# Optimization experiments

Measured on AMD Instinct MI355X. Metric: run time of the kernel, lower is better.

The kernel has to match this reference:

```python
import jax, jax.numpy as jnp
import numpy as np

EPS = 1e-5
NUM_HEADS = 4
TEMP = 0.1


def setup_inputs() -> dict:
    key = jax.random.key(0)
    ks = jax.random.split(key, 12)
    n, c, s, p, k = 64, 256, 64, 16, 4
    sc = 1.0 / np.sqrt(c)
    return {
        "x": jax.random.normal(ks[0], (n, c, s, p), dtype=jnp.float32),
        "prototypes": jax.random.normal(ks[1], (p, k, c), dtype=jnp.float32),
        "Wq": jax.random.normal(ks[2], (c, c), dtype=jnp.float32) * sc,
        "bq": jnp.zeros((c,), dtype=jnp.float32),
        "Wk": jax.random.normal(ks[3], (c, c), dtype=jnp.float32) * sc,
        "bk": jnp.zeros((c,), dtype=jnp.float32),
        "Wv": jax.random.normal(ks[4], (c, c), dtype=jnp.float32) * sc,
        "bv": jnp.zeros((c,), dtype=jnp.float32),
        "Wo": jax.random.normal(ks[5], (c, c), dtype=jnp.float32) * sc,
        "bo": jnp.zeros((c,), dtype=jnp.float32),
        "fc_bin": jax.random.normal(ks[6], (p, k * c, c), dtype=jnp.float32) * (1.0 / np.sqrt(k * c)),
    }


def _causal_attention(x, Wq, bq, Wk, bk, Wv, bv, Wo, bo):
    # x: (B, S, C) -> multi-head causal self-attention
    B, S, C = x.shape
    H = NUM_HEADS
    D = C // H
    q = (x @ Wq + bq).reshape(B, S, H, D).transpose(0, 2, 1, 3)
    k = (x @ Wk + bk).reshape(B, S, H, D).transpose(0, 2, 1, 3)
    v = (x @ Wv + bv).reshape(B, S, H, D).transpose(0, 2, 1, 3)
    scores = jnp.einsum('bhqd,bhkd->bhqk', q, k) / jnp.sqrt(jnp.float32(D))
    causal = jnp.tril(jnp.ones((S, S), dtype=bool))
    scores = jnp.where(causal, scores, jnp.finfo(scores.dtype).min)
    attn = jax.nn.softmax(scores, axis=-1)
    out = jnp.einsum('bhqk,bhkd->bhqd', attn, v)
    out = out.transpose(0, 2, 1, 3).reshape(B, S, C)
    return out @ Wo + bo


def reference(x, prototypes, Wq, bq, Wk, bk, Wv, bv, Wo, bo, fc_bin):
    n, c, s, p = x.shape
    kclusters = prototypes.shape[1]
    # n c s p -> p n s c
    x_part = x.transpose(3, 0, 2, 1)
    # InstanceNorm1d over the temporal (s) axis per (p, n, c)
    mu = x_part.mean(axis=2, keepdims=True)
    var = x_part.var(axis=2, keepdims=True)
    x_normed = (x_part - mu) / jnp.sqrt(var + EPS)
    # cosine similarity with prototypes
    xn = x_normed / jnp.linalg.norm(x_normed, axis=-1, keepdims=True)
    pn = prototypes / jnp.linalg.norm(prototypes, axis=-1, keepdims=True)
    sim = jnp.einsum('pnsc,pkc->pnsk', xn, pn)
    # straight-through hard/soft assignment (training=True path)
    soft = jax.nn.softmax(sim / TEMP, axis=-1)
    hard_idx = jnp.argmax(soft, axis=-1)                      # (p, n, s)
    hard = jax.nn.one_hot(hard_idx, kclusters, dtype=soft.dtype)
    assignment = jax.lax.stop_gradient(hard - soft) + soft    # (p, n, s, k)
    # mode over parts -> per-(n, s) cluster index
    idx_nsp = hard_idx.transpose(1, 2, 0)                     # (n, s, p)
    counts = jax.nn.one_hot(idx_nsp, kclusters, dtype=jnp.float32).sum(axis=2)
    cluster_indices = jnp.argmax(counts, axis=-1)             # (n, s)
    # causal attention with residual, batched over (n p)
    x2 = x.transpose(0, 3, 2, 1).reshape(n * p, s, c)         # (n p) s c
    x_attn = _causal_attention(x2, Wq, bq, Wk, bk, Wv, bv, Wo, bo) + x2
    x_attn = x_attn.reshape(n, p, s, c).transpose(1, 0, 2, 3)  # p n s c
    # scatter-max pooling: assignment-weighted max over time per cluster
    asg = assignment.transpose(0, 1, 3, 2)[..., None]         # (p, n, k, s, 1)
    grouped = asg * x_attn[:, :, None, :, :]                  # (p, n, k, s, c)
    clustered = grouped.max(axis=3)                           # (p, n, k, c)
    clustered = clustered.transpose(1, 2, 3, 0).reshape(n, kclusters * c, p)
    # SeparateFCs: per-part linear
    out = jnp.einsum('ncp,pco->nop', clustered, fc_bin)       # (n, c_out, p)
    return out, cluster_indices
```

## Files before the change

### kernel.cpp

```cpp
#include <hip/hip_runtime.h>

typedef unsigned short u16;
typedef unsigned int u32;
typedef __attribute__((ext_vector_type(8))) short bf16x8;
typedef __attribute__((ext_vector_type(4))) float f32x4;

typedef __attribute__((address_space(1))) const unsigned int gu32;
typedef __attribute__((address_space(3))) unsigned int lu32;

#define FMIN32 -3.402823466e38f

__device__ inline u16 f2bf(float f) {
    u32 x = __float_as_uint(f);
    u32 r = x + 0x7FFFu + ((x >> 16) & 1u);
    return (u16)(r >> 16);
}
__device__ inline float bf2f(u16 u) { return __uint_as_float(((u32)u) << 16); }

__device__ inline double wave_sum_d(double v) {
#pragma unroll
    for (int m = 1; m < 64; m <<= 1) v += __shfl_xor(v, m, 64);
    return v;
}

__global__ __launch_bounds__(256) void convert_w(const float* W0, const float* W1,
                                                 const float* W2, const float* W3, u16* Wt) {
    const float* Ws[4] = {W0, W1, W2, W3};
    int z = blockIdx.z;
    const float* W = Ws[z];
    u16* O = Wt + (size_t)z * 65536;
    __shared__ float tl[32][33];
    int t = threadIdx.x;
    int bx = blockIdx.x, by = blockIdx.y;
#pragma unroll
    for (int i = 0; i < 4; i++) {
        int e = i * 256 + t; int tr = e >> 5, tc = e & 31;
        tl[tr][tc] = W[(size_t)(bx * 32 + tr) * 256 + by * 32 + tc];
    }
    __syncthreads();
#pragma unroll
    for (int i = 0; i < 4; i++) {
        int e = i * 256 + t; int tr = e >> 5, tc = e & 31;
        O[(size_t)(by * 32 + tr) * 256 + bx * 32 + tc] = f2bf(tl[tc][tr]);
    }
}

__global__ __launch_bounds__(256) void convert_fc(const float* F, u16* O) {
    int p = blockIdx.z;
    int bx = blockIdx.x, by = blockIdx.y;
    const float* Fp = F + (size_t)p * 1024 * 256;
    u16* Op = O + (size_t)p * 256 * 1024;
    __shared__ float tl[32][33];
    int t = threadIdx.x;
#pragma unroll
    for (int i = 0; i < 4; i++) {
        int e = i * 256 + t; int tr = e >> 5, tc = e & 31;
        tl[tr][tc] = Fp[(size_t)(bx * 32 + tr) * 256 + by * 32 + tc];
    }
    __syncthreads();
#pragma unroll
    for (int i = 0; i < 4; i++) {
        int e = i * 256 + t; int tr = e >> 5, tc = e & 31;
        Op[(size_t)(by * 32 + tr) * 1024 + bx * 32 + tc] = f2bf(tl[tc][tr]);
    }
}

__global__ __launch_bounds__(256) void transpose_x(const float* x, float* xt, u16* xtbf) {
    int bx = blockIdx.x;
    int nn = bx >> 6, s = bx & 63;
    __shared__ float tile[16][257];
    int t = threadIdx.x;
    const float* xb = x + (size_t)nn * 262144 + (size_t)s * 16;
#pragma unroll
    for (int chunk = 0; chunk < 16; chunk++) {
        int e = chunk * 256 + t;
        int c = e >> 4, pp = e & 15;
        tile[pp][c] = xb[(size_t)c * 1024 + pp];
    }
    __syncthreads();
#pragma unroll
    for (int pp = 0; pp < 16; pp++) {
        float v = tile[pp][t];
        size_t o = ((size_t)(nn * 16 + pp) * 64 + s) * 256 + t;
        xt[o] = v;
        xtbf[o] = f2bf(v);
    }
}

__global__ __launch_bounds__(256) void norm_sim(const float* xt, const float* prot, int* hard) {
    int b = blockIdx.x;
    int pp = b & 15, nn = b >> 4;
    __shared__ float xs[64][257];
    __shared__ double wk[4][256];
    __shared__ double smu[256];
    __shared__ double srstd[256];
    __shared__ double offk[4];
    __shared__ double dd[64][5];
    int t = threadIdx.x, w = t >> 6, lane = t & 63;

    const float* xb = xt + (size_t)b * 64 * 256 + t;
    double s1 = 0.0, s2 = 0.0;
#pragma unroll 8
    for (int s = 0; s < 64; s++) {
        float v = xb[(size_t)s * 256];
        xs[s][t] = v;
        double dv = (double)v;
        s1 += dv; s2 += dv * dv;
    }
    double mu = s1 * (1.0 / 64.0);
    double var = s2 * (1.0 / 64.0) - mu * mu;
    smu[t] = mu;
    srstd[t] = 1.0 / sqrt(var + 1e-5);
    __syncthreads();

    {
        double pv[4]; double ss = 0.0;
#pragma unroll
        for (int j = 0; j < 4; j++) {
            pv[j] = (double)prot[((size_t)pp * 4 + w) * 256 + lane + 64 * j];
            ss += pv[j] * pv[j];
        }
        ss = wave_sum_d(ss);
        double rn = 1.0 / sqrt(ss);
        double po = 0.0;
#pragma unroll
        for (int j = 0; j < 4; j++) {
            int c = lane + 64 * j;
            double wv = pv[j] * rn * srstd[c];
            wk[w][c] = wv;
            po += wv * smu[c];
        }
        po = wave_sum_d(po);
        if (lane == 0) offk[w] = po;
    }
    __syncthreads();

    {
        int s = lane;
        const float* xr = &xs[s][0];
        const double* wr = &wk[w][0];
        double a0 = 0.0, a1 = 0.0, a2 = 0.0, a3 = 0.0;
#pragma unroll 8
        for (int c = 0; c < 256; c += 4) {
            a0 = fma((double)xr[c],     wr[c],     a0);
            a1 = fma((double)xr[c + 1], wr[c + 1], a1);
            a2 = fma((double)xr[c + 2], wr[c + 2], a2);
            a3 = fma((double)xr[c + 3], wr[c + 3], a3);
        }
        dd[s][w] = ((a0 + a1) + (a2 + a3)) - offk[w];
    }
    __syncthreads();

    if (t < 64) {
        double d0 = dd[t][0], d1 = dd[t][1], d2 = dd[t][2], d3 = dd[t][3];
        int best = 0; double bv = d0;
        if (d1 > bv) { bv = d1; best = 1; }
        if (d2 > bv) { bv = d2; best = 2; }
        if (d3 > bv) { best = 3; }
        hard[((pp * 64 + nn) << 6) + t] = best;
    }
}

__global__ __launch_bounds__(256) void cluster_mode(const int* hard, float* outp) {
    int tid = blockIdx.x * 256 + threadIdx.x;
    int nn = tid >> 6, s = tid & 63;
    int cnt[4] = {0, 0, 0, 0};
#pragma unroll
    for (int p = 0; p < 16; p++) cnt[hard[((p * 64 + nn) << 6) + s]]++;
    int best = 0;
#pragma unroll
    for (int k = 1; k < 4; k++) if (cnt[k] > cnt[best]) best = k;
    outp[tid] = (float)best;
}

__global__ __launch_bounds__(256, 2) void fused_attn(const u16* xtbf, const u16* Wt,
                                                  const float* bq, const float* bk, const float* bv,
                                                  const float* bo, const int* hard, u16* clus) {
    __shared__ u16 xs[64][264];
    __shared__ u16 scr[4][64][72];
    __shared__ int sidx[64];
    int t = threadIdx.x;
    int w = t >> 6, lane = t & 63;
    int l15 = lane & 15, qd = lane >> 4;
    int b = blockIdx.x;
    int pp = b & 15, nn = b >> 4;

    {
        const u16* xb = xtbf + (size_t)b * 16384;
#pragma unroll
        for (int i = 0; i < 8; i++) {
            int e = i * 256 + t;
            int r = e >> 5, g = e & 31;
            *(uint4*)&xs[r][g * 8] = *(const uint4*)(xb + (size_t)r * 256 + g * 8);
        }
        if (t < 64) sidx[t] = hard[((pp * 64 + nn) << 6) + t];
    }
    __syncthreads();

    const f32x4 zero4 = {0.f, 0.f, 0.f, 0.f};
    u16* sw = &scr[w][0][0];

    f32x4 accQ[4][4], accK[4][4];
#pragma unroll
    for (int mt = 0; mt < 4; mt++)
#pragma unroll
        for (int nt = 0; nt < 4; nt++) { accQ[mt][nt] = zero4; accK[mt][nt] = zero4; }
    {
        const u16* WQ = Wt + (size_t)(w * 64) * 256;
        const u16* WK = WQ + 65536;
#pragma unroll
        for (int kc = 0; kc < 8; kc++) {
            bf16x8 af[4], bq4[4], bk4[4];
#pragma unroll
            for (int mt = 0; mt < 4; mt++)
                af[mt] = *(const bf16x8*)(&xs[mt * 16 + l15][kc * 32 + qd * 8]);
#pragma unroll
            for (int nt = 0; nt < 4; nt++) {
                bq4[nt] = *(const bf16x8*)(WQ + (size_t)(nt * 16 + l15) * 256 + kc * 32 + qd * 8);
                bk4[nt] = *(const bf16x8*)(WK + (size_t)(nt * 16 + l15) * 256 + kc * 32 + qd * 8);
            }
#pragma unroll
            for (int mt = 0; mt < 4; mt++)
#pragma unroll
                for (int nt = 0; nt < 4; nt++) {
                    accQ[mt][nt] = __builtin_amdgcn_mfma_f32_16x16x32_bf16(af[mt], bq4[nt], accQ[mt][nt], 0, 0, 0);
                    accK[mt][nt] = __builtin_amdgcn_mfma_f32_16x16x32_bf16(af[mt], bk4[nt], accK[mt][nt], 0, 0, 0);
                }
        }
    }

    bf16x8 qf[2][4], kf[2][4];
#pragma unroll
    for (int mt = 0; mt < 4; mt++)
#pragma unroll
        for (int nt = 0; nt < 4; nt++) {
            int col = nt * 16 + l15;
            float bb = bq[w * 64 + col];
#pragma unroll
            for (int r = 0; r < 4; r++)
                sw[(mt * 16 + qd * 4 + r) * 72 + col] = f2bf(accQ[mt][nt][r] + bb);
        }
#pragma unroll
    for (int kc2 = 0; kc2 < 2; kc2++)
#pragma unroll
        for (int mt = 0; mt < 4; mt++)
            qf[kc2][mt] = *(const bf16x8*)(sw + (mt * 16 + l15) * 72 + kc2 * 32 + qd * 8);

#pragma unroll
    for (int mt = 0; mt < 4; mt++)
#pragma unroll
        for (int nt = 0; nt < 4; nt++) {
            int col = nt * 16 + l15;
            float bb = bk[w * 64 + col];
#pragma unroll
            for (int r = 0; r < 4; r++)
                sw[(mt * 16 + qd * 4 + r) * 72 + col] = f2bf(accK[mt][nt][r] + bb);
        }
#pragma unroll
    for (int kc2 = 0; kc2 < 2; kc2++)
#pragma unroll
        for (int mt = 0; mt < 4; mt++)
            kf[kc2][mt] = *(const bf16x8*)(sw + (mt * 16 + l15) * 72 + kc2 * 32 + qd * 8);

    f32x4 accS[4][4];
#pragma unroll
    for (int mt = 0; mt < 4; mt++)
#pragma unroll
        for (int nt = 0; nt < 4; nt++) accS[mt][nt] = zero4;
#pragma unroll
    for (int kc2 = 0; kc2 < 2; kc2++)
#pragma unroll
        for (int mt = 0; mt < 4; mt++)
#pragma unroll
            for (int nt = 0; nt < 4; nt++)
                accS[mt][nt] = __builtin_amdgcn_mfma_f32_16x16x32_bf16(qf[kc2][mt], kf[kc2][nt], accS[mt][nt], 0, 0, 0);

    f32x4 accV[4][4];
#pragma unroll
    for (int mt = 0; mt < 4; mt++)
#pragma unroll
        for (int nt = 0; nt < 4; nt++) accV[mt][nt] = zero4;
    {
        const u16* WV = Wt + 2 * 65536 + (size_t)(w * 64) * 256;
#pragma unroll
        for (int kc = 0; kc < 8; kc++) {
            bf16x8 af[4], bv4[4];
#pragma unroll
            for (int mt = 0; mt < 4; mt++)
                af[mt] = *(const bf16x8*)(&xs[mt * 16 + l15][kc * 32 + qd * 8]);
#pragma unroll
            for (int nt = 0; nt < 4; nt++)
                bv4[nt] = *(const bf16x8*)(WV + (size_t)(nt * 16 + l15) * 256 + kc * 32 + qd * 8);
#pragma unroll
            for (int mt = 0; mt < 4; mt++)
#pragma unroll
                for (int nt = 0; nt < 4; nt++)
                    accV[mt][nt] = __builtin_amdgcn_mfma_f32_16x16x32_bf16(af[mt], bv4[nt], accV[mt][nt], 0, 0, 0);
        }
    }

#pragma unroll
    for (int mt = 0; mt < 4; mt++) {
#pragma unroll
        for (int r = 0; r < 4; r++) {
            int row = mt * 16 + qd * 4 + r;
            float v[4];
#pragma unroll
            for (int nt = 0; nt < 4; nt++) {
                int col = nt * 16 + l15;
                float sv = accS[mt][nt][r] * 0.125f;
                if (col > row) sv = FMIN32;
                v[nt] = sv;
            }
            float m = fmaxf(fmaxf(v[0], v[1]), fmaxf(v[2], v[3]));
#pragma unroll
            for (int msk = 1; msk < 16; msk <<= 1) m = fmaxf(m, __shfl_xor(m, msk, 64));
            float e[4], ssum = 0.f;
#pragma unroll
            for (int nt = 0; nt < 4; nt++) { e[nt] = expf(v[nt] - m); ssum += e[nt]; }
#pragma unroll
            for (int msk = 1; msk < 16; msk <<= 1) ssum += __shfl_xor(ssum, msk, 64);
            float rinv = 1.0f / ssum;
#pragma unroll
            for (int nt = 0; nt < 4; nt++) sw[row * 72 + nt * 16 + l15] = f2bf(e[nt] * rinv);
        }
    }
    bf16x8 pf[2][4];
#pragma unroll
    for (int kc2 = 0; kc2 < 2; kc2++)
#pragma unroll
        for (int mt = 0; mt < 4; mt++)
            pf[kc2][mt] = *(const bf16x8*)(sw + (mt * 16 + l15) * 72 + kc2 * 32 + qd * 8);

#pragma unroll
    for (int mt = 0; mt < 4; mt++)
#pragma unroll
        for (int nt = 0; nt < 4; nt++) {
            int d = nt * 16 + l15;
            float bb = bv[w * 64 + d];
            ushort4 pk;
            pk.x = f2bf(accV[mt][nt][0] + bb);
            pk.y = f2bf(accV[mt][nt][1] + bb);
            pk.z = f2bf(accV[mt][nt][2] + bb);
            pk.w = f2bf(accV[mt][nt][3] + bb);
            *(ushort4*)(sw + d * 72 + mt * 16 + qd * 4) = pk;
        }
    bf16x8 vf[2][4];
#pragma unroll
    for (int kc2 = 0; kc2 < 2; kc2++)
#pragma unroll
        for (int nt = 0; nt < 4; nt++)
            vf[kc2][nt] = *(const bf16x8*)(sw + (nt * 16 + l15) * 72 + kc2 * 32 + qd * 8);

    f32x4 acc[4][4];
#pragma unroll
    for (int mt = 0; mt < 4; mt++)
#pragma unroll
        for (int nt = 0; nt < 4; nt++) acc[mt][nt] = zero4;
#pragma unroll
    for (int kc2 = 0; kc2 < 2; kc2++)
#pragma unroll
        for (int nt = 0; nt < 4; nt++)
#pragma unroll
            for (int mt = 0; mt < 4; mt++)
                acc[mt][nt] = __builtin_amdgcn_mfma_f32_16x16x32_bf16(pf[kc2][mt], vf[kc2][nt], acc[mt][nt], 0, 0, 0);

#pragma unroll
    for (int mt = 0; mt < 4; mt++)
#pragma unroll
        for (int nt = 0; nt < 4; nt++)
#pragma unroll
            for (int r = 0; r < 4; r++)
                sw[(mt * 16 + qd * 4 + r) * 72 + nt * 16 + l15] = f2bf(acc[mt][nt][r]);
    __syncthreads();

    {
        const u16* WO = Wt + 3 * 65536 + (size_t)(w * 64) * 256;
#pragma unroll
        for (int mt = 0; mt < 4; mt++)
#pragma unroll
            for (int nt = 0; nt < 4; nt++) acc[mt][nt] = zero4;
#pragma unroll
        for (int kc = 0; kc < 8; kc++) {
            int h = kc >> 1, k2 = kc & 1;
            bf16x8 af[4], bfr[4];
#pragma unroll
            for (int mt = 0; mt < 4; mt++)
                af[mt] = *(const bf16x8*)(&scr[h][mt * 16 + l15][k2 * 32 + qd * 8]);
#pragma unroll
            for (int nt = 0; nt < 4; nt++)
                bfr[nt] = *(const bf16x8*)(WO + (size_t)(nt * 16 + l15) * 256 + kc * 32 + qd * 8);
#pragma unroll
            for (int mt = 0; mt < 4; mt++)
#pragma unroll
                for (int nt = 0; nt < 4; nt++)
                    acc[mt][nt] = __builtin_amdgcn_mfma_f32_16x16x32_bf16(af[mt], bfr[nt], acc[mt][nt], 0, 0, 0);
        }
    }

#pragma unroll
    for (int mt = 0; mt < 4; mt++)
#pragma unroll
        for (int nt = 0; nt < 4; nt++) {
            int col = w * 64 + nt * 16 + l15;
            float bb = bo[col];
#pragma unroll
            for (int r = 0; r < 4; r++) {
                int s = mt * 16 + qd * 4 + r;
                acc[mt][nt][r] += bb + bf2f(xs[s][col]);
            }
        }
    int myidx = sidx[lane];
    u32 sr0 = 0, sr1 = 0;
#pragma unroll
    for (int mt = 0; mt < 4; mt++)
#pragma unroll
        for (int r = 0; r < 4; r++) {
            int idx = mt * 4 + r;
            u32 v = (u32)sidx[mt * 16 + qd * 4 + r];
            if (idx < 8) sr0 |= v << (idx * 4); else sr1 |= v << ((idx - 8) * 4);
        }
    size_t ob = ((size_t)(pp * 64 + nn)) * 1024;
#pragma unroll
    for (int k = 0; k < 4; k++) {
        unsigned long long bal = __ballot(myidx == k);
        int ck = __popcll(bal);
        float m0 = FMIN32, m1 = FMIN32, m2 = FMIN32, m3 = FMIN32;
#pragma unroll
        for (int mt = 0; mt < 4; mt++)
#pragma unroll
            for (int r = 0; r < 4; r++) {
                int idx = mt * 4 + r;
                u32 kk = ((idx < 8 ? sr0 : sr1) >> ((idx & 7) * 4)) & 15u;
                bool tk = (kk == (u32)k);
                m0 = tk ? fmaxf(m0, acc[mt][0][r]) : m0;
                m1 = tk ? fmaxf(m1, acc[mt][1][r]) : m1;
                m2 = tk ? fmaxf(m2, acc[mt][2][r]) : m2;
                m3 = tk ? fmaxf(m3, acc[mt][3][r]) : m3;
            }
        float mm[4] = {m0, m1, m2, m3};
#pragma unroll
        for (int nt = 0; nt < 4; nt++) {
            float m = mm[nt];
            m = fmaxf(m, __shfl_xor(m, 16, 64));
            m = fmaxf(m, __shfl_xor(m, 32, 64));
            if (ck < 64) m = fmaxf(m, 0.0f);
            if (qd == 0) clus[ob + k * 256 + w * 64 + nt * 16 + l15] = f2bf(m);
        }
    }
}

__global__ __launch_bounds__(256) void gemm_fc_mfma(const u16* clus, const u16* fcT, float* part) {
    int p = blockIdx.x, by = blockIdx.y, kz = blockIdx.z;
    __shared__ u16 As[64 * 32];
    __shared__ u16 Bs[64 * 32];
    const u16* Ap = clus + (size_t)p * 65536 + kz * 256;
    const u16* Bp = fcT + (size_t)p * 262144 + (size_t)(by * 64) * 1024 + kz * 256;
    int t = threadIdx.x;
    int w = t >> 6, lane = t & 63;
    int l15 = lane & 15, qd = lane >> 4;
    f32x4 acc[4] = {};
    int srow = t >> 2, scg = t & 3;
    for (int kc = 0; kc < 256; kc += 32) {
        *(uint4*)(As + srow * 32 + scg * 8) =
            *(const uint4*)(Ap + (size_t)srow * 1024 + kc + scg * 8);
        *(uint4*)(Bs + srow * 32 + scg * 8) =
            *(const uint4*)(Bp + (size_t)srow * 1024 + kc + scg * 8);
        __syncthreads();
        bf16x8 bfr = *(const bf16x8*)(Bs + (w * 16 + l15) * 32 + qd * 8);
#pragma unroll
        for (int mt = 0; mt < 4; mt++) {
            bf16x8 af = *(const bf16x8*)(As + (mt * 16 + l15) * 32 + qd * 8);
            acc[mt] = __builtin_amdgcn_mfma_f32_16x16x32_bf16(af, bfr, acc[mt], 0, 0, 0);
        }
        __syncthreads();
    }
#pragma unroll
    for (int mt = 0; mt < 4; mt++)
#pragma unroll
        for (int r = 0; r < 4; r++) {
            int n = mt * 16 + qd * 4 + r;
            int o = by * 64 + w * 16 + l15;
            part[(size_t)kz * 262144 + (size_t)n * 4096 + (size_t)o * 16 + p] = acc[mt][r];
        }
}

__global__ __launch_bounds__(256) void reduce_fc(const float* part, float* out) {
    int tid = blockIdx.x * 256 + threadIdx.x;
    const float4* p0 = (const float4*)part;
    float4 a = p0[tid];
    float4 b = p0[65536 + tid];
    float4 c = p0[131072 + tid];
    float4 d = p0[196608 + tid];
    float4 r;
    r.x = a.x + b.x + c.x + d.x;
    r.y = a.y + b.y + c.y + d.y;
    r.z = a.z + b.z + c.z + d.z;
    r.w = a.w + b.w + c.w + d.w;
    ((float4*)out)[tid] = r;
}

extern "C" void kernel_launch(void* const* d_in, const int* in_sizes, int n_in,
                              void* d_out, int out_size, void* d_ws, size_t ws_size,
                              hipStream_t stream) {
    const float* x    = (const float*)d_in[0];
    const float* prot = (const float*)d_in[1];
    const float* Wq   = (const float*)d_in[2];
    const float* bq   = (const float*)d_in[3];
    const float* Wk   = (const float*)d_in[4];
    const float* bk   = (const float*)d_in[5];
    const float* Wv   = (const float*)d_in[6];
    const float* bv   = (const float*)d_in[7];
    const float* Wo   = (const float*)d_in[8];
    const float* bo   = (const float*)d_in[9];
    const float* fcb  = (const float*)d_in[10];

    char* ws = (char*)d_ws;
    u16*   xtbf = (u16*)(ws + 0);
    float* xt   = (float*)(ws + 33554432);
    float* fcpart = (float*)(ws + 33554432);
    u16*   Wt   = (u16*)(ws + 134217728);
    u16*   fcT  = (u16*)(ws + 134742016);
    int*   hard = (int*)(ws + 143130624);
    u16*   clus = (u16*)(ws + 143392768);

    float* out_fc = (float*)d_out;
    float* out_ci = (float*)d_out + 262144;

    dim3 B(256);
    convert_w<<<dim3(8, 8, 4), B, 0, stream>>>(Wq, Wk, Wv, Wo, Wt);
    convert_fc<<<dim3(32, 8, 16), B, 0, stream>>>(fcb, fcT);
    transpose_x<<<dim3(4096), B, 0, stream>>>(x, xt, xtbf);
    norm_sim<<<dim3(1024), B, 0, stream>>>(xt, prot, hard);
    cluster_mode<<<dim3(16), B, 0, stream>>>(hard, out_ci);
    fused_attn<<<dim3(1024), B, 0, stream>>>(xtbf, Wt, bq, bk, bv, bo, hard, clus);
    gemm_fc_mfma<<<dim3(16, 4, 4), B, 0, stream>>>(clus, fcT, fcpart);
    reduce_fc<<<dim3(256), B, 0, stream>>>(fcpart, out_fc);
}
```

Before: 290.5 us.

## Split fused attention rows across two wave groups with 512-thread blocks

The fused attention kernel now runs 8 waves per block, with two groups each handling 32 of the 64 sequence rows for a head, halving per-wave accumulator arrays and register pressure. Shared scratch is shared between the groups, so extra barriers are inserted, and the per-cluster max pooling is combined across the two halves through shared memory before writing. The aim is more waves in flight per CU and better latency hiding, at the cost of more synchronisation and weight fragments loaded twice per block.

```diff
diff --git a/kernel.cpp b/kernel.cpp
--- a/kernel.cpp
+++ b/kernel.cpp
@@ -173,14 +173,18 @@
     outp[tid] = (float)best;
 }
 
-__global__ __launch_bounds__(256, 2) void fused_attn(const u16* xtbf, const u16* Wt,
+__global__ __launch_bounds__(512, 4) void fused_attn(const u16* xtbf, const u16* Wt,
                                                   const float* bq, const float* bk, const float* bv,
                                                   const float* bo, const int* hard, u16* clus) {
     __shared__ u16 xs[64][264];
     __shared__ u16 scr[4][64][72];
     __shared__ int sidx[64];
     int t = threadIdx.x;
-    int w = t >> 6, lane = t & 63;
+    int W = t >> 6;
+    int w = W & 3;
+    int h = W >> 2;
+    int rb = h * 32;
+    int lane = t & 63;
     int l15 = lane & 15, qd = lane >> 4;
     int b = blockIdx.x;
     int pp = b & 15, nn = b >> 4;
@@ -188,8 +192,8 @@
     {
         const u16* xb = xtbf + (size_t)b * 16384;
 #pragma unroll
-        for (int i = 0; i < 8; i++) {
-            int e = i * 256 + t;
+        for (int i = 0; i < 4; i++) {
+            int e = i * 512 + t;
             int r = e >> 5, g = e & 31;
             *(uint4*)&xs[r][g * 8] = *(const uint4*)(xb + (size_t)r * 256 + g * 8);
         }
@@ -200,9 +204,9 @@
     const f32x4 zero4 = {0.f, 0.f, 0.f, 0.f};
     u16* sw = &scr[w][0][0];
 
-    f32x4 accQ[4][4], accK[4][4];
-#pragma unroll
-    for (int mt = 0; mt < 4; mt++)
+    f32x4 accQ[2][4], accK[2][4];
+#pragma unroll
+    for (int mt = 0; mt < 2; mt++)
 #pragma unroll
         for (int nt = 0; nt < 4; nt++) { accQ[mt][nt] = zero4; accK[mt][nt] = zero4; }
     {
@@ -210,17 +214,17 @@
         const u16* WK = WQ + 65536;
 #pragma unroll
         for (int kc = 0; kc < 8; kc++) {
-            bf16x8 af[4], bq4[4], bk4[4];
-#pragma unroll
-            for (int mt = 0; mt < 4; mt++)
-                af[mt] = *(const bf16x8*)(&xs[mt * 16 + l15][kc * 32 + qd * 8]);
+            bf16x8 af[2], bq4[4], bk4[4];
+#pragma unroll
+            for (int mt = 0; mt < 2; mt++)
+                af[mt] = *(const bf16x8*)(&xs[rb + mt * 16 + l15][kc * 32 + qd * 8]);
 #pragma unroll
             for (int nt = 0; nt < 4; nt++) {
                 bq4[nt] = *(const bf16x8*)(WQ + (size_t)(nt * 16 + l15) * 256 + kc * 32 + qd * 8);
                 bk4[nt] = *(const bf16x8*)(WK + (size_t)(nt * 16 + l15) * 256 + kc * 32 + qd * 8);
             }
 #pragma unroll
-            for (int mt = 0; mt < 4; mt++)
+            for (int mt = 0; mt < 2; mt++)
 #pragma unroll
                 for (int nt = 0; nt < 4; nt++) {
                     accQ[mt][nt] = __builtin_amdgcn_mfma_f32_16x16x32_bf16(af[mt], bq4[nt], accQ[mt][nt], 0, 0, 0);
@@ -229,81 +233,83 @@
         }
     }
 
-    bf16x8 qf[2][4], kf[2][4];
-#pragma unroll
-    for (int mt = 0; mt < 4; mt++)
+    bf16x8 qf[2][2], kf[2][4];
+#pragma unroll
+    for (int mt = 0; mt < 2; mt++)
 #pragma unroll
         for (int nt = 0; nt < 4; nt++) {
             int col = nt * 16 + l15;
             float bb = bq[w * 64 + col];
 #pragma unroll
             for (int r = 0; r < 4; r++)
-                sw[(mt * 16 + qd * 4 + r) * 72 + col] = f2bf(accQ[mt][nt][r] + bb);
+                sw[(rb + mt * 16 + qd * 4 + r) * 72 + col] = f2bf(accQ[mt][nt][r] + bb);
         }
 #pragma unroll
     for (int kc2 = 0; kc2 < 2; kc2++)
 #pragma unroll
-        for (int mt = 0; mt < 4; mt++)
-            qf[kc2][mt] = *(const bf16x8*)(sw + (mt * 16 + l15) * 72 + kc2 * 32 + qd * 8);
-
-#pragma unroll
-    for (int mt = 0; mt < 4; mt++)
+        for (int mt = 0; mt < 2; mt++)
+            qf[kc2][mt] = *(const bf16x8*)(sw + (rb + mt * 16 + l15) * 72 + kc2 * 32 + qd * 8);
+
+#pragma unroll
+    for (int mt = 0; mt < 2; mt++)
 #pragma unroll
         for (int nt = 0; nt < 4; nt++) {
             int col = nt * 16 + l15;
             float bb = bk[w * 64 + col];
 #pragma unroll
             for (int r = 0; r < 4; r++)
-                sw[(mt * 16 + qd * 4 + r) * 72 + col] = f2bf(accK[mt][nt][r] + bb);
-        }
+                sw[(rb + mt * 16 + qd * 4 + r) * 72 + col] = f2bf(accK[mt][nt][r] + bb);
+        }
+    __syncthreads();
 #pragma unroll
     for (int kc2 = 0; kc2 < 2; kc2++)
 #pragma unroll
-        for (int mt = 0; mt < 4; mt++)
-            kf[kc2][mt] = *(const bf16x8*)(sw + (mt * 16 + l15) * 72 + kc2 * 32 + qd * 8);
-
-    f32x4 accS[4][4];
-#pragma unroll
-    for (int mt = 0; mt < 4; mt++)
+        for (int nt = 0; nt < 4; nt++)
+            kf[kc2][nt] = *(const bf16x8*)(sw + (nt * 16 + l15) * 72 + kc2 * 32 + qd * 8);
+
+    f32x4 accS[2][4];
+#pragma unroll
+    for (int mt = 0; mt < 2; mt++)
 #pragma unroll
         for (int nt = 0; nt < 4; nt++) accS[mt][nt] = zero4;
 #pragma unroll
     for (int kc2 = 0; kc2 < 2; kc2++)
 #pragma unroll
-        for (int mt = 0; mt < 4; mt++)
+        for (int mt = 0; mt < 2; mt++)
 #pragma unroll
             for (int nt = 0; nt < 4; nt++)
                 accS[mt][nt] = __builtin_amdgcn_mfma_f32_16x16x32_bf16(qf[kc2][mt], kf[kc2][nt], accS[mt][nt], 0, 0, 0);
 
-    f32x4 accV[4][4];
-#pragma unroll
-    for (int mt = 0; mt < 4; mt++)
+    f32x4 accV[2][4];
+#pragma unroll
+    for (int mt = 0; mt < 2; mt++)
 #pragma unroll
         for (int nt = 0; nt < 4; nt++) accV[mt][nt] = zero4;
     {
         const u16* WV = Wt + 2 * 65536 + (size_t)(w * 64) * 256;
 #pragma unroll
         for (int kc = 0; kc < 8; kc++) {
-            bf16x8 af[4], bv4[4];
-#pragma unroll
-            for (int mt = 0; mt < 4; mt++)
-                af[mt] = *(const bf16x8*)(&xs[mt * 16 + l15][kc * 32 + qd * 8]);
+            bf16x8 af[2], bv4[4];
+#pragma unroll
+            for (int mt = 0; mt < 2; mt++)
+                af[mt] = *(const bf16x8*)(&xs[rb + mt * 16 + l15][kc * 32 + qd * 8]);
 #pragma unroll
             for (int nt = 0; nt < 4; nt++)
                 bv4[nt] = *(const bf16x8*)(WV + (size_t)(nt * 16 + l15) * 256 + kc * 32 + qd * 8);
 #pragma unroll
-            for (int mt = 0; mt < 4; mt++)
+            for (int mt = 0; mt < 2; mt++)
 #pragma unroll
                 for (int nt = 0; nt < 4; nt++)
                     accV[mt][nt] = __builtin_amdgcn_mfma_f32_16x16x32_bf16(af[mt], bv4[nt], accV[mt][nt], 0, 0, 0);
         }
     }
-
-#pragma unroll
-    for (int mt = 0; mt < 4; mt++) {
+    __syncthreads();
+
+#pragma unroll
+    for (int mt = 0; mt < 2; mt++) {
 #pragma unroll
         for (int r = 0; r < 4; r++) {
-            int row = mt * 16 + qd * 4 + r;
+            int row = rb + mt * 16 + qd * 4 + r;
             float v[4];
 #pragma unroll
             for (int nt = 0; nt < 4; nt++) {
@@ -325,15 +331,16 @@
             for (int nt = 0; nt < 4; nt++) sw[row * 72 + nt * 16 + l15] = f2bf(e[nt] * rinv);
         }
     }
-    bf16x8 pf[2][4];
+    bf16x8 pf[2][2];
 #pragma unroll
     for (int kc2 = 0; kc2 < 2; kc2++)
 #pragma unroll
-        for (int mt = 0; mt < 4; mt++)
-            pf[kc2][mt] = *(const bf16x8*)(sw + (mt * 16 + l15) * 72 + kc2 * 32 + qd * 8);
-
-#pragma unroll
-    for (int mt = 0; mt < 4; mt++)
+        for (int mt = 0; mt < 2; mt++)
+            pf[kc2][mt] = *(const bf16x8*)(sw + (rb + mt * 16 + l15) * 72 + kc2 * 32 + qd * 8);
+    __syncthreads();
+
+#pragma unroll
+    for (int mt = 0; mt < 2; mt++)
 #pragma unroll
         for (int nt = 0; nt < 4; nt++) {
             int d = nt * 16 + l15;
@@ -343,18 +350,20 @@
             pk.y = f2bf(accV[mt][nt][1] + bb);
             pk.z = f2bf(accV[mt][nt][2] + bb);
             pk.w = f2bf(accV[mt][nt][3] + bb);
-            *(ushort4*)(sw + d * 72 + mt * 16 + qd * 4) = pk;
-        }
+            *(ushort4*)(sw + d * 72 + rb + mt * 16 + qd * 4) = pk;
+        }
+    __syncthreads();
     bf16x8 vf[2][4];
 #pragma unroll
     for (int kc2 = 0; kc2 < 2; kc2++)
 #pragma unroll
         for (int nt = 0; nt < 4; nt++)
             vf[kc2][nt] = *(const bf16x8*)(sw + (nt * 16 + l15) * 72 + kc2 * 32 + qd * 8);
-
-    f32x4 acc[4][4];
-#pragma unroll
-    for (int mt = 0; mt < 4; mt++)
+    __syncthreads();
+
+    f32x4 acc[2][4];
+#pragma unroll
+    for (int mt = 0; mt < 2; mt++)
 #pragma unroll
         for (int nt = 0; nt < 4; nt++) acc[mt][nt] = zero4;
 #pragma unroll
@@ -362,36 +371,36 @@
 #pragma unroll
         for (int nt = 0; nt < 4; nt++)
 #pragma unroll
-            for (int mt = 0; mt < 4; mt++)
+            for (int mt = 0; mt < 2; mt++)
                 acc[mt][nt] = __builtin_amdgcn_mfma_f32_16x16x32_bf16(pf[kc2][mt], vf[kc2][nt], acc[mt][nt], 0, 0, 0);
 
 #pragma unroll
-    for (int mt = 0; mt < 4; mt++)
+    for (int mt = 0; mt < 2; mt++)
 #pragma unroll
         for (int nt = 0; nt < 4; nt++)
 #pragma unroll
             for (int r = 0; r < 4; r++)
-                sw[(mt * 16 + qd * 4 + r) * 72 + nt * 16 + l15] = f2bf(acc[mt][nt][r]);
+                sw[(rb + mt * 16 + qd * 4 + r) * 72 + nt * 16 + l15] = f2bf(acc[mt][nt][r]);
     __syncthreads();
 
     {
         const u16* WO = Wt + 3 * 65536 + (size_t)(w * 64) * 256;
 #pragma unroll
-        for (int mt = 0; mt < 4; mt++)
+        for (int mt = 0; mt < 2; mt++)
 #pragma unroll
             for (int nt = 0; nt < 4; nt++) acc[mt][nt] = zero4;
 #pragma unroll
         for (int kc = 0; kc < 8; kc++) {
-            int h = kc >> 1, k2 = kc & 1;
-            bf16x8 af[4], bfr[4];
-#pragma unroll
-            for (int mt = 0; mt < 4; mt++)
-                af[mt] = *(const bf16x8*)(&scr[h][mt * 16 + l15][k2 * 32 + qd * 8]);
+            int hh = kc >> 1, k2 = kc & 1;
+            bf16x8 af[2], bfr[4];
+#pragma unroll
+            for (int mt = 0; mt < 2; mt++)
+                af[mt] = *(const bf16x8*)(&scr[hh][rb + mt * 16 + l15][k2 * 32 + qd * 8]);
 #pragma unroll
             for (int nt = 0; nt < 4; nt++)
                 bfr[nt] = *(const bf16x8*)(WO + (size_t)(nt * 16 + l15) * 256 + kc * 32 + qd * 8);
 #pragma unroll
-            for (int mt = 0; mt < 4; mt++)
+            for (int mt = 0; mt < 2; mt++)
 #pragma unroll
                 for (int nt = 0; nt < 4; nt++)
                     acc[mt][nt] = __builtin_amdgcn_mfma_f32_16x16x32_bf16(af[mt], bfr[nt], acc[mt][nt], 0, 0, 0);
@@ -399,39 +408,38 @@
     }
 
 #pragma unroll
-    for (int mt = 0; mt < 4; mt++)
+    for (int mt = 0; mt < 2; mt++)
 #pragma unroll
         for (int nt = 0; nt < 4; nt++) {
             int col = w * 64 + nt * 16 + l15;
             float bb = bo[col];
 #pragma unroll
             for (int r = 0; r < 4; r++) {
-                int s = mt * 16 + qd * 4 + r;
+                int s = rb + mt * 16 + qd * 4 + r;
                 acc[mt][nt][r] += bb + bf2f(xs[s][col]);
             }
         }
     int myidx = sidx[lane];
-    u32 sr0 = 0, sr1 = 0;
-#pragma unroll
-    for (int mt = 0; mt < 4; mt++)
-#pragma unroll
-        for (int r = 0; r < 4; r++) {
-            int idx = mt * 4 + r;
-            u32 v = (u32)sidx[mt * 16 + qd * 4 + r];
-            if (idx < 8) sr0 |= v << (idx * 4); else sr1 |= v << ((idx - 8) * 4);
-        }
-    size_t ob = ((size_t)(pp * 64 + nn)) * 1024;
+    u32 sr0 = 0;
+#pragma unroll
+    for (int mt = 0; mt < 2; mt++)
+#pragma unroll
+        for (int r = 0; r < 4; r++)
+            sr0 |= ((u32)sidx[rb + mt * 16 + qd * 4 + r]) << ((mt * 4 + r) * 4);
+
+    float* pbuf = (float*)(&scr[0][0][0]);
+    float pm[4][4];
+    int ckk[4];
 #pragma unroll
     for (int k = 0; k < 4; k++) {
         unsigned long long bal = __ballot(myidx == k);
-        int ck = __popcll(bal);
+        ckk[k] = __popcll(bal);
         float m0 = FMIN32, m1 = FMIN32, m2 = FMIN32, m3 = FMIN32;
 #pragma unroll
-        for (int mt = 0; mt < 4; mt++)
+        for (int mt = 0; mt < 2; mt++)
 #pragma unroll
             for (int r = 0; r < 4; r++) {
-                int idx = mt * 4 + r;
-                u32 kk = ((idx < 8 ? sr0 : sr1) >> ((idx & 7) * 4)) & 15u;
+                u32 kk = (sr0 >> ((mt * 4 + r) * 4)) & 15u;
                 bool tk = (kk == (u32)k);
                 m0 = tk ? fmaxf(m0, acc[mt][0][r]) : m0;
                 m1 = tk ? fmaxf(m1, acc[mt][1][r]) : m1;
@@ -444,9 +452,27 @@
             float m = mm[nt];
             m = fmaxf(m, __shfl_xor(m, 16, 64));
             m = fmaxf(m, __shfl_xor(m, 32, 64));
-            if (ck < 64) m = fmaxf(m, 0.0f);
-            if (qd == 0) clus[ob + k * 256 + w * 64 + nt * 16 + l15] = f2bf(m);
-        }
+            if (ckk[k] < 64) m = fmaxf(m, 0.0f);
+            pm[k][nt] = m;
+        }
+    }
+    __syncthreads();
+#pragma unroll
+    for (int k = 0; k < 4; k++)
+#pragma unroll
+        for (int nt = 0; nt < 4; nt++)
+            if (qd == 0) pbuf[(h * 4 + k) * 256 + w * 64 + nt * 16 + l15] = pm[k][nt];
+    __syncthreads();
+    if (h == 0) {
+        size_t ob = ((size_t)(pp * 64 + nn)) * 1024;
+#pragma unroll
+        for (int k = 0; k < 4; k++)
+#pragma unroll
+            for (int nt = 0; nt < 4; nt++) {
+                int col = w * 64 + nt * 16 + l15;
+                float m = fmaxf(pbuf[k * 256 + col], pbuf[(4 + k) * 256 + col]);
+                if (qd == 0) clus[ob + k * 256 + col] = f2bf(m);
+            }
     }
 }
 
@@ -533,7 +559,7 @@
     transpose_x<<<dim3(4096), B, 0, stream>>>(x, xt, xtbf);
     norm_sim<<<dim3(1024), B, 0, stream>>>(xt, prot, hard);
     cluster_mode<<<dim3(16), B, 0, stream>>>(hard, out_ci);
-    fused_attn<<<dim3(1024), B, 0, stream>>>(xtbf, Wt, bq, bk, bv, bo, hard, clus);
+    fused_attn<<<dim3(1024), dim3(512), 0, stream>>>(xtbf, Wt, bq, bk, bv, bo, hard, clus);
     gemm_fc_mfma<<<dim3(16, 4, 4), B, 0, stream>>>(clus, fcT, fcpart);
     reduce_fc<<<dim3(256), B, 0, stream>>>(fcpart, out_fc);
 }
```

After: 346.4 us. +19.2%, slower.
